# Kernel optimization log

Measured on AMD Instinct MI355X. Metric: run time of the kernel, lower is better.

Reference implementation:

```python
import jax, jax.numpy as jnp
import numpy as np

B, N, D = 2, 2048, 1024
H, HD = 16, 64


def setup_inputs() -> dict:
    key = jax.random.key(0)
    ks = jax.random.split(key, 5)
    return {
        "hidden_states": jax.random.normal(ks[0], (B, N, D), dtype=jnp.float32),
        "W_attn": jax.random.normal(ks[1], (D, 3 * D), dtype=jnp.float32) * (D ** -0.5),
        "b_attn": jax.random.normal(ks[2], (3 * D,), dtype=jnp.float32) * 0.02,
        "W_proj": jax.random.normal(ks[3], (D, D), dtype=jnp.float32) * (D ** -0.5),
        "b_proj": jax.random.normal(ks[4], (D,), dtype=jnp.float32) * 0.02,
    }


def reference(hidden_states, W_attn, b_attn, W_proj, b_proj):
    # QKV projection: [B,N,3D]
    proj = hidden_states @ W_attn + b_attn
    q, k, v = jnp.split(proj, 3, axis=-1)
    # [B,N,H,HD]
    q = q.reshape(B, N, H, HD)
    k = k.reshape(B, N, H, HD)
    v = v.reshape(B, N, H, HD)
    scale = HD ** -0.5
    # naive attention: full [B,H,Nq,Nkv] score matrix
    attn = jnp.einsum("bqhd,bkhd->bhqk", q, k) * scale
    q_pos = jnp.arange(N)
    kv_pos = jnp.arange(N)
    # mask where kv_pos > start_pos + q_pos (start_pos = 0)
    mask = kv_pos[None, :] > q_pos[:, None]  # [Nq, Nkv]
    attn = jnp.where(mask[None, None, :, :], -jnp.inf, attn)
    attn = jax.nn.softmax(attn, axis=-1)
    out = jnp.einsum("bhqk,bkhd->bqhd", attn, v)  # [B,N,H,HD]
    out = out.reshape(B, N, D)
    return out @ W_proj + b_proj
```

## Files before the change

### kernel.cpp

```cpp
#include <hip/hip_runtime.h>
#include <hip/hip_bf16.h>

#define BB 2
#define NN 2048
#define DDIM 1024
#define HH 16
#define HDD 64

typedef __attribute__((ext_vector_type(8))) short bf16x8;
typedef __attribute__((ext_vector_type(4))) short bf16x4;
typedef __attribute__((ext_vector_type(4))) float f32x4;

__device__ inline ushort f2bf(float x) {
  __hip_bfloat16 h = __float2bfloat16(x);
  ushort u;
  __builtin_memcpy(&u, &h, 2);
  return u;
}
__device__ inline float bf2f(ushort u) {
  unsigned v = (unsigned)u << 16;
  float f;
  __builtin_memcpy(&f, &v, 4);
  return f;
}
__device__ inline float exp2_raw(float x) {
  float r;
  asm("v_exp_f32 %0, %1" : "=v"(r) : "v"(x));
  return r;
}

#define GLOAD_LDS16(g, l)                                                              \
  __builtin_amdgcn_global_load_lds((const __attribute__((address_space(1))) void*)(g), \
                                   (__attribute__((address_space(3))) void*)(l), 16, 0, 0)

__global__ __launch_bounds__(256) void prep(const float* __restrict__ hidden,
                                            const float* __restrict__ W_attn,
                                            const float* __restrict__ W_proj,
                                            ushort* __restrict__ hbf,
                                            ushort* __restrict__ WaT,
                                            ushort* __restrict__ WpT) {
  __shared__ float tile[32][33];
  const int bid = blockIdx.x, tid = threadIdx.x;
  if (bid < 2048) {
    int i = bid * 256 + tid;
    const float4* in4 = (const float4*)hidden;
#pragma unroll
    for (int r = 0; r < 2; ++r, i += 524288) {
      float4 a = in4[i];
      ushort4 o;
      o.x = f2bf(a.x); o.y = f2bf(a.y); o.z = f2bf(a.z); o.w = f2bf(a.w);
      ((ushort4*)hbf)[i] = o;
    }
    return;
  }
  const float* in;
  ushort* out;
  int R, C, bx, by;
  if (bid < 2048 + 3072) {
    int b2 = bid - 2048;
    in = W_attn; out = WaT; R = 1024; C = 3072;
    bx = (b2 % 96) * 32; by = (b2 / 96) * 32;
  } else {
    int b3 = bid - 2048 - 3072;
    in = W_proj; out = WpT; R = 1024; C = 1024;
    bx = (b3 & 31) * 32; by = (b3 >> 5) * 32;
  }
  const int tx = tid & 31, ty = tid >> 5;
#pragma unroll
  for (int r = ty; r < 32; r += 8)
    tile[r][tx] = in[(size_t)(by + r) * C + bx + tx];
  __syncthreads();
#pragma unroll
  for (int r = ty; r < 32; r += 8)
    out[(size_t)(bx + r) * R + by + tx] = f2bf(tile[tx][r]);
}

template <int MODE>
__global__ __launch_bounds__(256) void gemm_bt(const ushort* __restrict__ A,
                                               const ushort* __restrict__ Bt,
                                               const float* __restrict__ bias,
                                               void* __restrict__ Cv,
                                               ushort* __restrict__ Vt,
                                               int M, int N, int K) {
  __shared__ ushort As[128 * 32];
  __shared__ ushort Bs[128 * 32];
  const int tid = threadIdx.x;
  const int wid = tid >> 6, lane = tid & 63;
  const int c = lane & 15, g = lane >> 4;
  const int wm = (wid >> 1) * 64, wn = (wid & 1) * 64;
  const int m0 = blockIdx.y * 128, n0 = blockIdx.x * 128;
  f32x4 acc[4][4] = {};
  for (int k0 = 0; k0 < K; k0 += 32) {
    __syncthreads();
#pragma unroll
    for (int it = 0; it < 2; ++it) {
      int G = tid + it * 256;
      int row = G >> 2, sl = G & 3;
      GLOAD_LDS16(A + (size_t)(m0 + row) * K + k0 + sl * 8, &As[G * 8]);
      GLOAD_LDS16(Bt + (size_t)(n0 + row) * K + k0 + sl * 8, &Bs[G * 8]);
    }
    __syncthreads();
    bf16x8 af[4], bfr[4];
#pragma unroll
    for (int i = 0; i < 4; ++i) {
      af[i] = *(const bf16x8*)(&As[(wm + i * 16 + c) * 32 + g * 8]);
      bfr[i] = *(const bf16x8*)(&Bs[(wn + i * 16 + c) * 32 + g * 8]);
    }
#pragma unroll
    for (int i = 0; i < 4; ++i)
#pragma unroll
      for (int j = 0; j < 4; ++j)
        acc[i][j] = __builtin_amdgcn_mfma_f32_16x16x32_bf16(af[i], bfr[j], acc[i][j], 0, 0, 0);
  }
#pragma unroll
  for (int i = 0; i < 4; ++i) {
#pragma unroll
    for (int j = 0; j < 4; ++j) {
      const int col = n0 + wn + j * 16 + c;
      const float bv = bias[col];
      const int row = m0 + wm + i * 16 + g * 4;
      if (MODE == 2 && col >= 2048) {
        const int hh = (col - 2048) >> 6, dd = (col - 2048) & 63;
        const int bb = row >> 11, nl = row & 2047;
        ushort4 ov;
        ov.x = f2bf(acc[i][j][0] + bv);
        ov.y = f2bf(acc[i][j][1] + bv);
        ov.z = f2bf(acc[i][j][2] + bv);
        ov.w = f2bf(acc[i][j][3] + bv);
        *(ushort4*)(&Vt[(size_t)((bb * 16 + hh) * 64 + dd) * NN + nl]) = ov;
      } else {
        const int ldc = (MODE == 2) ? 2048 : N;
#pragma unroll
        for (int ri = 0; ri < 4; ++ri) {
          float v = acc[i][j][ri] + bv;
          ((ushort*)Cv)[(size_t)(row + ri) * ldc + col] = f2bf(v);
        }
      }
    }
  }
}

__global__ __launch_bounds__(256) void gemm_proj(const ushort* __restrict__ A,
                                                 const ushort* __restrict__ Bt,
                                                 const float* __restrict__ bias,
                                                 float* __restrict__ C, int M, int N, int K) {
  __shared__ ushort As[64 * 32];
  __shared__ ushort Bs[128 * 32];
  const int tid = threadIdx.x;
  const int wid = tid >> 6, lane = tid & 63;
  const int c = lane & 15, g = lane >> 4;
  const int wn = wid * 32;
  const int m0 = blockIdx.y * 64, n0 = blockIdx.x * 128;
  f32x4 acc[4][2] = {};
  for (int k0 = 0; k0 < K; k0 += 32) {
    __syncthreads();
#pragma unroll
    for (int it = 0; it < 3; ++it) {
      int G = tid + it * 256;
      if (G < 256) {
        int row = G >> 2, sl = G & 3;
        GLOAD_LDS16(A + (size_t)(m0 + row) * K + k0 + sl * 8, &As[G * 8]);
      } else {
        int GB = G - 256;
        int row = GB >> 2, sl = GB & 3;
        GLOAD_LDS16(Bt + (size_t)(n0 + row) * K + k0 + sl * 8, &Bs[GB * 8]);
      }
    }
    __syncthreads();
    bf16x8 af[4], bfr[2];
#pragma unroll
    for (int i = 0; i < 4; ++i) af[i] = *(const bf16x8*)(&As[(i * 16 + c) * 32 + g * 8]);
#pragma unroll
    for (int j = 0; j < 2; ++j)
      bfr[j] = *(const bf16x8*)(&Bs[(wn + j * 16 + c) * 32 + g * 8]);
#pragma unroll
    for (int i = 0; i < 4; ++i)
#pragma unroll
      for (int j = 0; j < 2; ++j)
        acc[i][j] = __builtin_amdgcn_mfma_f32_16x16x32_bf16(af[i], bfr[j], acc[i][j], 0, 0, 0);
  }
#pragma unroll
  for (int i = 0; i < 4; ++i) {
#pragma unroll
    for (int j = 0; j < 2; ++j) {
      const int col = n0 + wn + j * 16 + c;
      const float bv = bias[col];
      const int row = m0 + i * 16 + g * 4;
#pragma unroll
      for (int ri = 0; ri < 4; ++ri)
        C[(size_t)(row + ri) * N + col] = acc[i][j][ri] + bv;
    }
  }
}

__global__ __launch_bounds__(512) void attn_fwd(const ushort* __restrict__ QK,
                                                const ushort* __restrict__ Vt,
                                                ushort* __restrict__ O,
                                                ushort* __restrict__ partO,
                                                float* __restrict__ partML) {
  const int bh = blockIdx.x;
  const int b = bh >> 4, h = bh & 15;
  const int y = blockIdx.y;
  int qb, t_lo, t_hi, half;
  bool split;
  if (y < 8) {
    qb = y; t_lo = 0; t_hi = 2 * qb + 2; half = 0; split = false;
  } else {
    int u = y - 8;
    qb = 8 + (u >> 1); half = u & 1; split = true;
    int mid = qb + 1;
    t_lo = half ? mid : 0;
    t_hi = half ? (2 * qb + 2) : mid;
  }
  const int tid = threadIdx.x;
  const int wid = tid >> 6, lane = tid & 63;
  const int c = lane & 15, g = lane >> 4;
  const int q0 = qb * 128 + wid * 16;
  const ushort* Qb = QK + (size_t)b * NN * 2048 + (size_t)h * HDD;
  const ushort* Kb = Qb + 1024;
  const ushort* Vb = Vt + (size_t)bh * HDD * NN;

  __shared__ ushort Ks[2][64 * 64];
  __shared__ ushort Vs[2][64 * 64];

  const float SC = 0.18033688011112042f;
  bf16x8 qf[2];
  {
    const ushort* qrow = Qb + (size_t)(q0 + c) * 2048 + g * 8;
    qf[0] = *(const bf16x8*)(qrow);
    qf[1] = *(const bf16x8*)(qrow + 32);
#pragma unroll
    for (int r = 0; r < 2; ++r)
#pragma unroll
      for (int e = 0; e < 8; ++e) qf[r][e] = (short)f2bf(bf2f((ushort)qf[r][e]) * SC);
  }

  f32x4 oacc[4] = {};
  float m = 0.f, lsum = 0.f;
  const int q_abs = q0 + c;
  const int tdiag = 2 * qb + (wid >> 2);

#define STAGE_TILE(kv0, bufi)                                                   \
  do {                                                                          \
    int u = tid;                                                                \
    int row = u >> 3, sl = u & 7;                                               \
    int ksl = (sl ^ (row & 7)) * 8;                                             \
    GLOAD_LDS16(Kb + (size_t)((kv0) + row) * 2048 + ksl, &Ks[bufi][u * 8]);     \
    GLOAD_LDS16(Vb + (size_t)row * NN + (kv0) + ksl, &Vs[bufi][u * 8]);         \
  } while (0)

  STAGE_TILE(t_lo * 64, 0);
  __syncthreads();
  int cur = 0;

  for (int t = t_lo; t < t_hi; ++t) {
    if (t + 1 < t_hi) STAGE_TILE((t + 1) * 64, cur ^ 1);

    if (t <= tdiag) {
      f32x4 s[4] = {};
#pragma unroll
      for (int f = 0; f < 4; ++f) {
        int krow = f * 16 + c;
#pragma unroll
        for (int dc = 0; dc < 2; ++dc) {
          int slot = (dc * 4 + g) ^ (krow & 7);
          bf16x8 kf = *(const bf16x8*)(&Ks[cur][krow * 64 + slot * 8]);
          s[f] = __builtin_amdgcn_mfma_f32_16x16x32_bf16(kf, qf[dc], s[f], 0, 0, 0);
        }
      }

      float pmax = -INFINITY;
      if (t == tdiag) {
        const int kv0 = t * 64;
#pragma unroll
        for (int f = 0; f < 4; ++f)
#pragma unroll
          for (int i = 0; i < 4; ++i) {
            if (kv0 + f * 16 + g * 4 + i > q_abs) s[f][i] = -INFINITY;
            pmax = fmaxf(pmax, s[f][i]);
          }
      } else {
#pragma unroll
        for (int f = 0; f < 4; ++f)
#pragma unroll
          for (int i = 0; i < 4; ++i) pmax = fmaxf(pmax, s[f][i]);
      }

      if (t == t_lo) {
        float pr = fmaxf(pmax, __shfl_xor(pmax, 16));
        pr = fmaxf(pr, __shfl_xor(pr, 32));
        m = pr;
      } else if (!__all(pmax <= m + 8.f)) {
        float pr = fmaxf(pmax, __shfl_xor(pmax, 16));
        pr = fmaxf(pr, __shfl_xor(pr, 32));
        float mnew = fmaxf(m, pr);
        float corr = exp2_raw(m - mnew);
        lsum *= corr;
#pragma unroll
        for (int db = 0; db < 4; ++db) {
          oacc[db][0] *= corr; oacc[db][1] *= corr;
          oacc[db][2] *= corr; oacc[db][3] *= corr;
        }
        m = mnew;
      }

      float psum = 0.f;
#pragma unroll
      for (int f = 0; f < 4; ++f)
#pragma unroll
        for (int i = 0; i < 4; ++i) {
          float p = exp2_raw(s[f][i] - m);
          s[f][i] = p;
          psum += p;
        }
      lsum += psum;

#pragma unroll
      for (int f = 0; f < 4; ++f) {
        bf16x4 pb;
        pb[0] = (short)f2bf(s[f][0]);
        pb[1] = (short)f2bf(s[f][1]);
        pb[2] = (short)f2bf(s[f][2]);
        pb[3] = (short)f2bf(s[f][3]);
        const int slot = f * 2 + (g >> 1);
#pragma unroll
        for (int db = 0; db < 4; ++db) {
          int d = db * 16 + c;
          bf16x4 vf =
              *(const bf16x4*)(&Vs[cur][d * 64 + ((slot ^ (d & 7)) * 8) + (g & 1) * 4]);
          oacc[db] = __builtin_amdgcn_mfma_f32_16x16x16bf16_1k(vf, pb, oacc[db], 0, 0, 0);
        }
      }
    }
    __syncthreads();
    cur ^= 1;
  }

  lsum += __shfl_xor(lsum, 16);
  lsum += __shfl_xor(lsum, 32);

  if (!split) {
    float invl = 1.f / lsum;
    ushort* orow = O + (size_t)(b * NN + q0 + c) * DDIM + h * HDD;
#pragma unroll
    for (int db = 0; db < 4; ++db) {
      ushort4 ov;
      ov.x = f2bf(oacc[db][0] * invl);
      ov.y = f2bf(oacc[db][1] * invl);
      ov.z = f2bf(oacc[db][2] * invl);
      ov.w = f2bf(oacc[db][3] * invl);
      *(ushort4*)(&orow[db * 16 + g * 4]) = ov;
    }
  } else {
    const int e = (((bh << 3) + (qb - 8)) << 1) + half;
    const int ql = wid * 16 + c;
    if (g == 0) {
      partML[(size_t)e * 256 + ql] = m;
      partML[(size_t)e * 256 + 128 + ql] = lsum;
    }
    ushort* po = partO + (size_t)e * 8192 + ql * 64;
#pragma unroll
    for (int db = 0; db < 4; ++db) {
      ushort4 ov;
      ov.x = f2bf(oacc[db][0]);
      ov.y = f2bf(oacc[db][1]);
      ov.z = f2bf(oacc[db][2]);
      ov.w = f2bf(oacc[db][3]);
      *(ushort4*)(&po[db * 16 + g * 4]) = ov;
    }
  }
}

__global__ __launch_bounds__(256) void attn_combine(const ushort* __restrict__ partO,
                                                    const float* __restrict__ partML,
                                                    ushort* __restrict__ O) {
  const int bh = blockIdx.x, qb8 = blockIdx.y;
  const int b = bh >> 4, h = bh & 15;
  const int tid = threadIdx.x;
  const int q = tid & 127, dh = tid >> 7;
  const int e0 = (((bh << 3) + qb8) << 1), e1 = e0 + 1;
  const float ma = partML[(size_t)e0 * 256 + q], la = partML[(size_t)e0 * 256 + 128 + q];
  const float mb = partML[(size_t)e1 * 256 + q], lb = partML[(size_t)e1 * 256 + 128 + q];
  const float mm = fmaxf(ma, mb);
  const float wa = exp2_raw(ma - mm), wb = exp2_raw(mb - mm);
  const float inv = 1.f / (la * wa + lb * wb);
  const ushort* pa = partO + (size_t)e0 * 8192 + q * 64 + dh * 32;
  const ushort* pc = partO + (size_t)e1 * 8192 + q * 64 + dh * 32;
  const int qg = (8 + qb8) * 128 + q;
  ushort* out = O + (size_t)(b * NN + qg) * DDIM + h * HDD + dh * 32;
#pragma unroll
  for (int j0 = 0; j0 < 32; j0 += 8) {
    bf16x8 va = *(const bf16x8*)(pa + j0);
    bf16x8 vb = *(const bf16x8*)(pc + j0);
    bf16x8 vo;
#pragma unroll
    for (int e = 0; e < 8; ++e)
      vo[e] = (short)f2bf((bf2f((ushort)va[e]) * wa + bf2f((ushort)vb[e]) * wb) * inv);
    *(bf16x8*)(out + j0) = vo;
  }
}

extern "C" void kernel_launch(void* const* d_in, const int* in_sizes, int n_in,
                              void* d_out, int out_size, void* d_ws, size_t ws_size,
                              hipStream_t stream) {
  const float* hidden = (const float*)d_in[0];
  const float* W_attn = (const float*)d_in[1];
  const float* b_attn = (const float*)d_in[2];
  const float* W_proj = (const float*)d_in[3];
  const float* b_proj = (const float*)d_in[4];

  char* ws = (char*)d_ws;
  ushort* hbf  = (ushort*)(ws);
  ushort* WaT  = (ushort*)(ws + (size_t)(8 << 20));
  ushort* WpT  = (ushort*)(ws + (size_t)(14 << 20));
  ushort* qk   = (ushort*)(ws + (size_t)(16 << 20));
  ushort* vt   = (ushort*)(ws + (size_t)(32 << 20));
  ushort* aout = (ushort*)(ws + (size_t)(40 << 20));
  ushort* partO  = (ushort*)(ws);
  float*  partML = (float*)(ws + (size_t)(8 << 20));

  prep<<<2048 + 3072 + 1024, 256, 0, stream>>>(hidden, W_attn, W_proj, hbf, WaT, WpT);
  gemm_bt<2><<<dim3(24, 32), 256, 0, stream>>>(hbf, WaT, b_attn, qk, vt, 4096, 3072, 1024);
  attn_fwd<<<dim3(32, 24), 512, 0, stream>>>(qk, vt, aout, partO, partML);
  attn_combine<<<dim3(32, 8), 256, 0, stream>>>(partO, partML, aout);
  gemm_proj<<<dim3(8, 64), 256, 0, stream>>>(aout, WpT, b_proj, (float*)d_out, 4096, 1024, 1024);
}
```

Baseline: 191.6 us.

## Process two 128-row query groups per attention block to reuse K/V tiles

Each attention workgroup now handles 256 query rows as two register-resident 128-row groups. Every staged K/V tile in LDS feeds MFMAs for both groups, which halves LDS staging and global K/V traffic per query row. The grid drops from 24 to 14 blocks per head, and the split/combine scheme is remapped so the six largest query blocks are split in half. The costs are doubled accumulator and score register pressure, fewer blocks for load balance, and partial-buffer offsets that move in the workspace.

```diff
diff --git a/kernel.cpp b/kernel.cpp
--- a/kernel.cpp
+++ b/kernel.cpp
@@ -201,21 +201,18 @@
   const int bh = blockIdx.x;
   const int b = bh >> 4, h = bh & 15;
   const int y = blockIdx.y;
-  int qb, t_lo, t_hi, half;
+  int qb, half;
   bool split;
-  if (y < 8) {
-    qb = y; t_lo = 0; t_hi = 2 * qb + 2; half = 0; split = false;
-  } else {
-    int u = y - 8;
-    qb = 8 + (u >> 1); half = u & 1; split = true;
-    int mid = qb + 1;
-    t_lo = half ? mid : 0;
-    t_hi = half ? (2 * qb + 2) : mid;
-  }
+  if (y < 12) { qb = 7 - (y >> 1); half = y & 1; split = true; }
+  else        { qb = 13 - y;       half = 0;     split = false; }
+  const int ntile = 4 * qb + 4, mid = 2 * qb + 2;
+  const int t_lo = (split && half) ? mid : 0;
+  const int t_hi = (split && !half) ? mid : ntile;
+
   const int tid = threadIdx.x;
   const int wid = tid >> 6, lane = tid & 63;
   const int c = lane & 15, g = lane >> 4;
-  const int q0 = qb * 128 + wid * 16;
+  const int q0 = qb * 256 + wid * 16;
   const ushort* Qb = QK + (size_t)b * NN * 2048 + (size_t)h * HDD;
   const ushort* Kb = Qb + 1024;
   const ushort* Vb = Vt + (size_t)bh * HDD * NN;
@@ -224,21 +221,23 @@
   __shared__ ushort Vs[2][64 * 64];
 
   const float SC = 0.18033688011112042f;
-  bf16x8 qf[2];
-  {
-    const ushort* qrow = Qb + (size_t)(q0 + c) * 2048 + g * 8;
-    qf[0] = *(const bf16x8*)(qrow);
-    qf[1] = *(const bf16x8*)(qrow + 32);
-#pragma unroll
-    for (int r = 0; r < 2; ++r)
-#pragma unroll
-      for (int e = 0; e < 8; ++e) qf[r][e] = (short)f2bf(bf2f((ushort)qf[r][e]) * SC);
-  }
-
-  f32x4 oacc[4] = {};
-  float m = 0.f, lsum = 0.f;
-  const int q_abs = q0 + c;
-  const int tdiag = 2 * qb + (wid >> 2);
+  bf16x8 qf[2][2];
+#pragma unroll
+  for (int r = 0; r < 2; ++r) {
+    const ushort* qrow = Qb + (size_t)(q0 + r * 128 + c) * 2048 + g * 8;
+    qf[r][0] = *(const bf16x8*)(qrow);
+    qf[r][1] = *(const bf16x8*)(qrow + 32);
+#pragma unroll
+    for (int dc = 0; dc < 2; ++dc)
+#pragma unroll
+      for (int e = 0; e < 8; ++e)
+        qf[r][dc][e] = (short)f2bf(bf2f((ushort)qf[r][dc][e]) * SC);
+  }
+
+  f32x4 oacc[2][4] = {};
+  float m[2] = {0.f, 0.f}, lsum[2] = {0.f, 0.f};
+  const int q_abs[2] = {q0 + c, q0 + 128 + c};
+  const int tdiag[2] = {4 * qb + (wid >> 2), 4 * qb + 2 + (wid >> 2)};
 
 #define STAGE_TILE(kv0, bufi)                                                   \
   do {                                                                          \
@@ -255,118 +254,129 @@
 
   for (int t = t_lo; t < t_hi; ++t) {
     if (t + 1 < t_hi) STAGE_TILE((t + 1) * 64, cur ^ 1);
-
-    if (t <= tdiag) {
-      f32x4 s[4] = {};
-#pragma unroll
-      for (int f = 0; f < 4; ++f) {
-        int krow = f * 16 + c;
-#pragma unroll
-        for (int dc = 0; dc < 2; ++dc) {
-          int slot = (dc * 4 + g) ^ (krow & 7);
-          bf16x8 kf = *(const bf16x8*)(&Ks[cur][krow * 64 + slot * 8]);
-          s[f] = __builtin_amdgcn_mfma_f32_16x16x32_bf16(kf, qf[dc], s[f], 0, 0, 0);
-        }
-      }
-
+    const bool act0 = (t <= tdiag[0]);
+    const bool act1 = (t <= tdiag[1]);
+
+    f32x4 s[2][4] = {};
+#pragma unroll
+    for (int f = 0; f < 4; ++f) {
+      int krow = f * 16 + c;
+#pragma unroll
+      for (int dc = 0; dc < 2; ++dc) {
+        int slot = (dc * 4 + g) ^ (krow & 7);
+        bf16x8 kf = *(const bf16x8*)(&Ks[cur][krow * 64 + slot * 8]);
+        if (act0) s[0][f] = __builtin_amdgcn_mfma_f32_16x16x32_bf16(kf, qf[0][dc], s[0][f], 0, 0, 0);
+        if (act1) s[1][f] = __builtin_amdgcn_mfma_f32_16x16x32_bf16(kf, qf[1][dc], s[1][f], 0, 0, 0);
+      }
+    }
+
+    bf16x4 pb[2][4];
+#pragma unroll
+    for (int r = 0; r < 2; ++r) {
+      const bool act = r ? act1 : act0;
+      if (!act) continue;
       float pmax = -INFINITY;
-      if (t == tdiag) {
+      if (t == tdiag[r]) {
         const int kv0 = t * 64;
 #pragma unroll
         for (int f = 0; f < 4; ++f)
 #pragma unroll
           for (int i = 0; i < 4; ++i) {
-            if (kv0 + f * 16 + g * 4 + i > q_abs) s[f][i] = -INFINITY;
-            pmax = fmaxf(pmax, s[f][i]);
+            if (kv0 + f * 16 + g * 4 + i > q_abs[r]) s[r][f][i] = -INFINITY;
+            pmax = fmaxf(pmax, s[r][f][i]);
           }
       } else {
 #pragma unroll
         for (int f = 0; f < 4; ++f)
 #pragma unroll
-          for (int i = 0; i < 4; ++i) pmax = fmaxf(pmax, s[f][i]);
-      }
-
+          for (int i = 0; i < 4; ++i) pmax = fmaxf(pmax, s[r][f][i]);
+      }
       if (t == t_lo) {
         float pr = fmaxf(pmax, __shfl_xor(pmax, 16));
         pr = fmaxf(pr, __shfl_xor(pr, 32));
-        m = pr;
-      } else if (!__all(pmax <= m + 8.f)) {
+        m[r] = pr;
+      } else if (!__all(pmax <= m[r] + 8.f)) {
         float pr = fmaxf(pmax, __shfl_xor(pmax, 16));
         pr = fmaxf(pr, __shfl_xor(pr, 32));
-        float mnew = fmaxf(m, pr);
-        float corr = exp2_raw(m - mnew);
-        lsum *= corr;
+        float mnew = fmaxf(m[r], pr);
+        float corr = exp2_raw(m[r] - mnew);
+        lsum[r] *= corr;
 #pragma unroll
         for (int db = 0; db < 4; ++db) {
-          oacc[db][0] *= corr; oacc[db][1] *= corr;
-          oacc[db][2] *= corr; oacc[db][3] *= corr;
+          oacc[r][db][0] *= corr; oacc[r][db][1] *= corr;
+          oacc[r][db][2] *= corr; oacc[r][db][3] *= corr;
         }
-        m = mnew;
-      }
-
+        m[r] = mnew;
+      }
       float psum = 0.f;
 #pragma unroll
-      for (int f = 0; f < 4; ++f)
+      for (int f = 0; f < 4; ++f) {
 #pragma unroll
         for (int i = 0; i < 4; ++i) {
-          float p = exp2_raw(s[f][i] - m);
-          s[f][i] = p;
+          float p = exp2_raw(s[r][f][i] - m[r]);
+          s[r][f][i] = p;
           psum += p;
         }
-      lsum += psum;
-
-#pragma unroll
-      for (int f = 0; f < 4; ++f) {
-        bf16x4 pb;
-        pb[0] = (short)f2bf(s[f][0]);
-        pb[1] = (short)f2bf(s[f][1]);
-        pb[2] = (short)f2bf(s[f][2]);
-        pb[3] = (short)f2bf(s[f][3]);
-        const int slot = f * 2 + (g >> 1);
-#pragma unroll
-        for (int db = 0; db < 4; ++db) {
-          int d = db * 16 + c;
-          bf16x4 vf =
-              *(const bf16x4*)(&Vs[cur][d * 64 + ((slot ^ (d & 7)) * 8) + (g & 1) * 4]);
-          oacc[db] = __builtin_amdgcn_mfma_f32_16x16x16bf16_1k(vf, pb, oacc[db], 0, 0, 0);
-        }
+        pb[r][f][0] = (short)f2bf(s[r][f][0]);
+        pb[r][f][1] = (short)f2bf(s[r][f][1]);
+        pb[r][f][2] = (short)f2bf(s[r][f][2]);
+        pb[r][f][3] = (short)f2bf(s[r][f][3]);
+      }
+      lsum[r] += psum;
+    }
+
+#pragma unroll
+    for (int f = 0; f < 4; ++f) {
+      const int slot = f * 2 + (g >> 1);
+#pragma unroll
+      for (int db = 0; db < 4; ++db) {
+        int d = db * 16 + c;
+        bf16x4 vf =
+            *(const bf16x4*)(&Vs[cur][d * 64 + ((slot ^ (d & 7)) * 8) + (g & 1) * 4]);
+        if (act0)
+          oacc[0][db] = __builtin_amdgcn_mfma_f32_16x16x16bf16_1k(vf, pb[0][f], oacc[0][db], 0, 0, 0);
+        if (act1)
+          oacc[1][db] = __builtin_amdgcn_mfma_f32_16x16x16bf16_1k(vf, pb[1][f], oacc[1][db], 0, 0, 0);
       }
     }
     __syncthreads();
     cur ^= 1;
   }
 
-  lsum += __shfl_xor(lsum, 16);
-  lsum += __shfl_xor(lsum, 32);
-
-  if (!split) {
-    float invl = 1.f / lsum;
-    ushort* orow = O + (size_t)(b * NN + q0 + c) * DDIM + h * HDD;
-#pragma unroll
-    for (int db = 0; db < 4; ++db) {
-      ushort4 ov;
-      ov.x = f2bf(oacc[db][0] * invl);
-      ov.y = f2bf(oacc[db][1] * invl);
-      ov.z = f2bf(oacc[db][2] * invl);
-      ov.w = f2bf(oacc[db][3] * invl);
-      *(ushort4*)(&orow[db * 16 + g * 4]) = ov;
-    }
-  } else {
-    const int e = (((bh << 3) + (qb - 8)) << 1) + half;
-    const int ql = wid * 16 + c;
-    if (g == 0) {
-      partML[(size_t)e * 256 + ql] = m;
-      partML[(size_t)e * 256 + 128 + ql] = lsum;
-    }
-    ushort* po = partO + (size_t)e * 8192 + ql * 64;
-#pragma unroll
-    for (int db = 0; db < 4; ++db) {
-      ushort4 ov;
-      ov.x = f2bf(oacc[db][0]);
-      ov.y = f2bf(oacc[db][1]);
-      ov.z = f2bf(oacc[db][2]);
-      ov.w = f2bf(oacc[db][3]);
-      *(ushort4*)(&po[db * 16 + g * 4]) = ov;
+#pragma unroll
+  for (int r = 0; r < 2; ++r) {
+    float l = lsum[r];
+    l += __shfl_xor(l, 16);
+    l += __shfl_xor(l, 32);
+    if (!split) {
+      float invl = 1.f / l;
+      ushort* orow = O + (size_t)(b * NN + q0 + r * 128 + c) * DDIM + h * HDD;
+#pragma unroll
+      for (int db = 0; db < 4; ++db) {
+        ushort4 ov;
+        ov.x = f2bf(oacc[r][db][0] * invl);
+        ov.y = f2bf(oacc[r][db][1] * invl);
+        ov.z = f2bf(oacc[r][db][2] * invl);
+        ov.w = f2bf(oacc[r][db][3] * invl);
+        *(ushort4*)(&orow[db * 16 + g * 4]) = ov;
+      }
+    } else {
+      const int e = (bh * 6 + (qb - 2)) * 2 + half;
+      const int ql = r * 128 + wid * 16 + c;
+      if (g == 0) {
+        partML[(size_t)e * 512 + ql] = m[r];
+        partML[(size_t)e * 512 + 256 + ql] = l;
+      }
+      ushort* po = partO + (size_t)e * 16384 + ql * 64;
+#pragma unroll
+      for (int db = 0; db < 4; ++db) {
+        ushort4 ov;
+        ov.x = f2bf(oacc[r][db][0]);
+        ov.y = f2bf(oacc[r][db][1]);
+        ov.z = f2bf(oacc[r][db][2]);
+        ov.w = f2bf(oacc[r][db][3]);
+        *(ushort4*)(&po[db * 16 + g * 4]) = ov;
+      }
     }
   }
 }
@@ -374,22 +384,21 @@
 __global__ __launch_bounds__(256) void attn_combine(const ushort* __restrict__ partO,
                                                     const float* __restrict__ partML,
                                                     ushort* __restrict__ O) {
-  const int bh = blockIdx.x, qb8 = blockIdx.y;
+  const int bh = blockIdx.x, qb = 2 + blockIdx.y;
   const int b = bh >> 4, h = bh & 15;
-  const int tid = threadIdx.x;
-  const int q = tid & 127, dh = tid >> 7;
-  const int e0 = (((bh << 3) + qb8) << 1), e1 = e0 + 1;
-  const float ma = partML[(size_t)e0 * 256 + q], la = partML[(size_t)e0 * 256 + 128 + q];
-  const float mb = partML[(size_t)e1 * 256 + q], lb = partML[(size_t)e1 * 256 + 128 + q];
+  const int q = threadIdx.x;
+  const int e0 = (bh * 6 + (qb - 2)) * 2, e1 = e0 + 1;
+  const float ma = partML[(size_t)e0 * 512 + q], la = partML[(size_t)e0 * 512 + 256 + q];
+  const float mb = partML[(size_t)e1 * 512 + q], lb = partML[(size_t)e1 * 512 + 256 + q];
   const float mm = fmaxf(ma, mb);
   const float wa = exp2_raw(ma - mm), wb = exp2_raw(mb - mm);
   const float inv = 1.f / (la * wa + lb * wb);
-  const ushort* pa = partO + (size_t)e0 * 8192 + q * 64 + dh * 32;
-  const ushort* pc = partO + (size_t)e1 * 8192 + q * 64 + dh * 32;
-  const int qg = (8 + qb8) * 128 + q;
-  ushort* out = O + (size_t)(b * NN + qg) * DDIM + h * HDD + dh * 32;
-#pragma unroll
-  for (int j0 = 0; j0 < 32; j0 += 8) {
+  const ushort* pa = partO + (size_t)e0 * 16384 + q * 64;
+  const ushort* pc = partO + (size_t)e1 * 16384 + q * 64;
+  const int qg = qb * 256 + q;
+  ushort* out = O + (size_t)(b * NN + qg) * DDIM + h * HDD;
+#pragma unroll
+  for (int j0 = 0; j0 < 64; j0 += 8) {
     bf16x8 va = *(const bf16x8*)(pa + j0);
     bf16x8 vb = *(const bf16x8*)(pc + j0);
     bf16x8 vo;
@@ -417,11 +426,11 @@
   ushort* vt   = (ushort*)(ws + (size_t)(32 << 20));
   ushort* aout = (ushort*)(ws + (size_t)(40 << 20));
   ushort* partO  = (ushort*)(ws);
-  float*  partML = (float*)(ws + (size_t)(8 << 20));
+  float*  partML = (float*)(ws + (size_t)(12 << 20));
 
   prep<<<2048 + 3072 + 1024, 256, 0, stream>>>(hidden, W_attn, W_proj, hbf, WaT, WpT);
   gemm_bt<2><<<dim3(24, 32), 256, 0, stream>>>(hbf, WaT, b_attn, qk, vt, 4096, 3072, 1024);
-  attn_fwd<<<dim3(32, 24), 512, 0, stream>>>(qk, vt, aout, partO, partML);
-  attn_combine<<<dim3(32, 8), 256, 0, stream>>>(partO, partML, aout);
+  attn_fwd<<<dim3(32, 14), 512, 0, stream>>>(qk, vt, aout, partO, partML);
+  attn_combine<<<dim3(32, 6), 256, 0, stream>>>(partO, partML, aout);
   gemm_proj<<<dim3(8, 64), 256, 0, stream>>>(aout, WpT, b_proj, (float*)d_out, 4096, 1024, 1024);
 }
```

After: 206.7 us. 1.08x slower.
